# Performance work log

Hardware: AMD Instinct MI355X
Metric: run time of the kernel (lower is better)

The kernel has to match this reference:

```python
import jax, jax.numpy as jnp
import numpy as np

N = 50000   # nodes per graph
E = 1600000 # edges per graph
F = 1024    # literal feature dim (hardcoded in source)
D = 256     # gcn_dims
B = 16384   # ent_ids batch
NUM_HOPS = 3
SLOPE = 0.01  # nn.LeakyReLU default


def spmm(row, col, val, X):
    # sparse [N,N] @ X[N,F] via COO gather + segment-sum
    return jax.ops.segment_sum(val[:, None] * X[col], row, num_segments=N)


def gcn(row, col, val, X, W, b):
    return jax.nn.leaky_relu(spmm(row, col, val, X) @ W + b, SLOPE)


def setup_inputs() -> dict:
    key = jax.random.key(0)
    ks = jax.random.split(key, 24)
    d = {}
    d['ent_lit'] = jax.random.normal(ks[0], (N, F), jnp.float32)
    d['rel_lit'] = jax.random.normal(ks[1], (N, F), jnp.float32)
    d['attr_lit'] = jax.random.normal(ks[2], (N, F), jnp.float32)
    d['ent_val'] = jax.random.uniform(ks[3], (E,), jnp.float32)
    d['rel_val'] = jax.random.uniform(ks[4], (E,), jnp.float32)
    d['attr_val'] = jax.random.uniform(ks[5], (E,), jnp.float32)
    s_in = 1.0 / np.sqrt(F)
    s_d = 1.0 / np.sqrt(D)
    d['W_ent'] = jax.random.normal(ks[6], (F, D), jnp.float32) * s_in
    d['b_ent'] = jnp.zeros((D,), jnp.float32)
    d['W_rel'] = jax.random.normal(ks[7], (F, D), jnp.float32) * s_in
    d['b_rel'] = jnp.zeros((D,), jnp.float32)
    d['W_attr'] = jax.random.normal(ks[8], (F, D), jnp.float32) * s_in
    d['b_attr'] = jnp.zeros((D,), jnp.float32)
    d['W_x'] = jax.random.normal(ks[9], (D, D), jnp.float32) * s_d
    d['b_x'] = jnp.zeros((D,), jnp.float32)
    d['W_lit'] = jax.random.normal(ks[10], (F, D), jnp.float32) * s_in
    d['b_lit'] = jnp.zeros((D,), jnp.float32)
    d['W_gate'] = jax.random.normal(ks[11], (D, D), jnp.float32) * s_d
    d['b_gate'] = jnp.zeros((D,), jnp.float32)
    d['ent_row'] = jax.random.randint(ks[12], (E,), 0, N, jnp.int32)
    d['ent_col'] = jax.random.randint(ks[13], (E,), 0, N, jnp.int32)
    d['rel_row'] = jax.random.randint(ks[14], (E,), 0, N, jnp.int32)
    d['rel_col'] = jax.random.randint(ks[15], (E,), 0, N, jnp.int32)
    d['attr_row'] = jax.random.randint(ks[16], (E,), 0, N, jnp.int32)
    d['attr_col'] = jax.random.randint(ks[17], (E,), 0, N, jnp.int32)
    d['ent_ids'] = jax.random.randint(ks[18], (B,), 0, N, jnp.int32)
    return d


def reference(ent_lit, rel_lit, attr_lit, ent_val, rel_val, attr_val,
              W_ent, b_ent, W_rel, b_rel, W_attr, b_attr, W_x, b_x,
              W_lit, b_lit, W_gate, b_gate,
              ent_row, ent_col, rel_row, rel_col, attr_row, attr_col, ent_ids):
    rel_repr = gcn(rel_row, rel_col, rel_val, rel_lit, W_rel, b_rel)[ent_ids]
    attr_repr = gcn(attr_row, attr_col, attr_val, attr_lit, W_attr, b_attr)[ent_ids]
    ent_literals = ent_lit[ent_ids] @ W_lit + b_lit
    # n-hop gated aggregation
    h = gcn(ent_row, ent_col, ent_val, ent_lit, W_ent, b_ent)
    for _ in range(1, NUM_HOPS):
        nxt = jax.nn.leaky_relu(spmm(ent_row, ent_col, ent_val, h) @ W_x + b_x, SLOPE)
        g = jax.nn.sigmoid(h @ W_gate + b_gate)
        h = g * nxt + (1.0 - g) * h
    ent_n_hop = h[ent_ids]
    return jnp.concatenate([ent_literals, ent_n_hop, rel_repr, attr_repr], axis=1)
```

## Files before the change

### kernel.cpp

```cpp
#include <hip/hip_runtime.h>
#include <math.h>

#define N_NODES 50000
#define N_EDGES 1600000
#define F_DIM 1024
#define D_DIM 256
#define B_IDS 16384

#define BROWS 1024
#define BKT 49
#define NB3 (3 * BKT)
#define CHUNK 4096

typedef __attribute__((ext_vector_type(8))) short bf16x8;
typedef __attribute__((ext_vector_type(4))) float f32x4;

static inline size_t alignup(size_t x) { return (x + 255) & ~(size_t)255; }

__device__ inline unsigned short f2bf(float f) {
  unsigned u = __float_as_uint(f);
  u += 0x7fffu + ((u >> 16) & 1u);
  return (unsigned short)(u >> 16);
}
__device__ inline float bf2f(unsigned short u) {
  return __uint_as_float(((unsigned)u) << 16);
}

__device__ inline void glds16(const void* g, void* l) {
  __builtin_amdgcn_global_load_lds(
      (const __attribute__((address_space(1))) void*)g,
      (__attribute__((address_space(3))) void*)l, 16, 0, 0);
}

struct TrArgs {
  const float* W[6];
  unsigned short* Wh[6];
  unsigned short* Wl[6];
  int K[6];
};

__global__ __launch_bounds__(256) void tr_all_k(TrArgs a) {
  const int z = blockIdx.z;
  const int K = a.K[z];
  if (blockIdx.x * 64 >= K) return;
  const float* W = a.W[z];
  unsigned short* Wt_hi = a.Wh[z];
  unsigned short* Wt_lo = a.Wl[z];
  __shared__ float t[64][65];
  const int k0 = blockIdx.x * 64, n0 = blockIdx.y * 64;
  const int tid = threadIdx.x;
  const int rr = tid >> 4, c4 = (tid & 15) * 4;
#pragma unroll
  for (int q = 0; q < 4; ++q) {
    int row = q * 16 + rr;
    const float4 v = *reinterpret_cast<const float4*>(W + (size_t)(k0 + row) * 256 + n0 + c4);
    t[row][c4 + 0] = v.x; t[row][c4 + 1] = v.y; t[row][c4 + 2] = v.z; t[row][c4 + 3] = v.w;
  }
  __syncthreads();
#pragma unroll
  for (int q = 0; q < 4; ++q) {
    int n = q * 16 + rr;
    ushort4 oh, ol;
    float w0 = t[c4 + 0][n], w1 = t[c4 + 1][n], w2 = t[c4 + 2][n], w3 = t[c4 + 3][n];
    oh.x = f2bf(w0); ol.x = f2bf(w0 - bf2f(oh.x));
    oh.y = f2bf(w1); ol.y = f2bf(w1 - bf2f(oh.y));
    oh.z = f2bf(w2); ol.z = f2bf(w2 - bf2f(oh.z));
    oh.w = f2bf(w3); ol.w = f2bf(w3 - bf2f(oh.w));
    *reinterpret_cast<ushort4*>(Wt_hi + (size_t)(n0 + n) * K + k0 + c4) = oh;
    *reinterpret_cast<ushort4*>(Wt_lo + (size_t)(n0 + n) * K + k0 + c4) = ol;
  }
}


__global__ __launch_bounds__(256) void bcount_k(
    const int* __restrict__ r0, const int* __restrict__ r1, const int* __restrict__ r2,
    int* __restrict__ bcnt)
{
  __shared__ int h[NB3];
  const int t = threadIdx.x;
  for (int i = t; i < NB3; i += 256) h[i] = 0;
  __syncthreads();
  const long long cbase = (long long)blockIdx.x * CHUNK;
  const long long tot = 3LL * N_EDGES;
#pragma unroll
  for (int j = 0; j < 16; ++j) {
    long long idx = cbase + j * 256 + t;
    if (idx < tot) {
      int g = (int)(idx / N_EDGES);
      int e = (int)(idx - (long long)g * N_EDGES);
      int row = (g == 0 ? r0 : g == 1 ? r1 : r2)[e];
      atomicAdd(&h[g * BKT + (row >> 10)], 1);
    }
  }
  __syncthreads();
  for (int i = t; i < NB3; i += 256)
    if (h[i]) atomicAdd(&bcnt[i], h[i]);
}

__global__ void bscan_k(const int* __restrict__ bcnt, int* __restrict__ flatBase,
                        int* __restrict__ cursor) {
  __shared__ int c[NB3];
  const int t = threadIdx.x;
  if (t < NB3) c[t] = bcnt[t];
  __syncthreads();
  if (t < 3) {
    int acc = t * N_EDGES;
    for (int b = 0; b < BKT; ++b) {
      int i = t * BKT + b;
      int v = c[i];
      flatBase[i] = acc;
      cursor[i] = acc;
      acc += v;
    }
  }
  if (t == 0) flatBase[NB3] = 3 * N_EDGES;
}

__global__ __launch_bounds__(256) void bpart_k(
    const int* __restrict__ r0, const int* __restrict__ c0, const float* __restrict__ v0,
    const int* __restrict__ r1, const int* __restrict__ c1, const float* __restrict__ v1,
    const int* __restrict__ r2, const int* __restrict__ c2, const float* __restrict__ v2,
    int* __restrict__ cursor, int2* __restrict__ packed)
{
  __shared__ int hs[256];
  __shared__ int ls[NB3];
  __shared__ int cur[NB3];
  __shared__ int clm[NB3];
  __shared__ int2 stg[CHUNK];
  __shared__ int tgt[CHUNK];
  const int t = threadIdx.x;
  const long long cbase = (long long)blockIdx.x * CHUNK;
  const long long tot = 3LL * N_EDGES;
  hs[t] = 0;
  __syncthreads();
  int rows_[16], gbs_[16];
#pragma unroll
  for (int j = 0; j < 16; ++j) {
    long long idx = cbase + j * 256 + t;
    int gb = -1, row = 0;
    if (idx < tot) {
      int g = (int)(idx / N_EDGES);
      int e = (int)(idx - (long long)g * N_EDGES);
      row = (g == 0 ? r0 : g == 1 ? r1 : r2)[e];
      gb = g * BKT + (row >> 10);
      atomicAdd(&hs[gb], 1);
    }
    gbs_[j] = gb; rows_[j] = row;
  }
  __syncthreads();
  const int myh = hs[t];
  if (t < NB3) clm[t] = atomicAdd(&cursor[t], myh);
  for (int off = 1; off < 256; off <<= 1) {
    int v = (t >= off) ? hs[t - off] : 0;
    __syncthreads();
    hs[t] += v;
    __syncthreads();
  }
  const int excl = hs[t] - myh;
  if (t < NB3) { ls[t] = excl; cur[t] = excl; }
  __syncthreads();
#pragma unroll
  for (int j = 0; j < 16; ++j) {
    const int gb = gbs_[j];
    if (gb >= 0) {
      long long idx = cbase + j * 256 + t;
      int g = (int)(idx / N_EDGES);
      int e = (int)(idx - (long long)g * N_EDGES);
      int col = (g == 0 ? c0 : g == 1 ? c1 : c2)[e];
      float vv = (g == 0 ? v0 : g == 1 ? v1 : v2)[e];
      int slot = atomicAdd(&cur[gb], 1);
      stg[slot] = make_int2(rows_[j] | (col << 16), __float_as_int(vv));
      tgt[slot] = clm[gb] + (slot - ls[gb]);
    }
  }
  __syncthreads();
  const int cnt = (int)min((long long)CHUNK, tot - cbase);
  for (int i = t; i < cnt; i += 256) packed[tgt[i]] = stg[i];
}

__global__ __launch_bounds__(256) void bfinal_k(
    const int2* __restrict__ packed, const int* __restrict__ flatBase,
    int* __restrict__ row_ptr3, int2* __restrict__ cv3)
{
  __shared__ int hist[BROWS];
  __shared__ int part[256];
  const int gb = blockIdx.x;
  const int g = gb / BKT, b = gb % BKT;
  const int rb = b * BROWS;
  const int nrows = min(BROWS, N_NODES - rb);
  const int base = flatBase[gb];
  const int cnt = flatBase[gb + 1] - base;
  const int cvb = base - g * N_EDGES;
  const int t = threadIdx.x;
  for (int i = t; i < BROWS; i += 256) hist[i] = 0;
  __syncthreads();
  for (int i = t; i < cnt; i += 256) {
    int rc = packed[base + i].x;
    atomicAdd(&hist[(rc & 0xffff) - rb], 1);
  }
  __syncthreads();
  const int l0 = hist[4 * t], l1 = hist[4 * t + 1], l2 = hist[4 * t + 2], l3 = hist[4 * t + 3];
  const int s = l0 + l1 + l2 + l3;
  part[t] = s;
  __syncthreads();
  for (int off = 1; off < 256; off <<= 1) {
    int v = (t >= off) ? part[t - off] : 0;
    __syncthreads();
    part[t] += v;
    __syncthreads();
  }
  const int pexcl = part[t] - s;
  const int e0 = pexcl, e1 = e0 + l0, e2 = e1 + l1, e3 = e2 + l2;
  hist[4 * t] = e0; hist[4 * t + 1] = e1; hist[4 * t + 2] = e2; hist[4 * t + 3] = e3;
  int* rp = row_ptr3 + (size_t)g * (N_NODES + 1);
  if (4 * t + 0 < nrows) rp[rb + 4 * t + 0] = cvb + e0;
  if (4 * t + 1 < nrows) rp[rb + 4 * t + 1] = cvb + e1;
  if (4 * t + 2 < nrows) rp[rb + 4 * t + 2] = cvb + e2;
  if (4 * t + 3 < nrows) rp[rb + 4 * t + 3] = cvb + e3;
  if (rb + BROWS >= N_NODES && t == 0) rp[N_NODES] = N_EDGES;
  __syncthreads();
  for (int i = t; i < cnt; i += 256) {
    int2 p = packed[base + i];
    int row = p.x & 0xffff;
    int col = ((unsigned)p.x) >> 16;
    int pos = atomicAdd(&hist[row - rb], 1);
    cv3[base + pos] = make_int2(col, p.y);
  }
}

__global__ void flag_k(const int* __restrict__ ids, unsigned char* __restrict__ flag, int B) {
  int i = blockIdx.x * blockDim.x + threadIdx.x;
  if (i < B) flag[ids[i]] = 1;
}

__global__ __launch_bounds__(256) void spmm_k(
    const int* __restrict__ row_ptr, const int2* __restrict__ cv,
    const unsigned short* __restrict__ srcb, float* __restrict__ dst,
    unsigned short* __restrict__ dstb,
    const float* __restrict__ bias, int do_leaky,
    const unsigned char* __restrict__ flag, int n)
{
  int r = (blockIdx.x << 2) + (threadIdx.x >> 6);
  if (r >= n) return;
  if (flag && !flag[r]) return;
  const int lane = threadIdx.x & 63;
  const int c0 = lane << 2;
  int e0 = row_ptr[r], e1 = row_ptr[r + 1];
  float a0 = 0.f, a1 = 0.f, a2 = 0.f, a3 = 0.f;
  int e = e0;
  for (; e + 3 < e1; e += 4) {
    int2 p0 = cv[e], p1 = cv[e + 1], p2 = cv[e + 2], p3 = cv[e + 3];
    const ushort4 x0 = *reinterpret_cast<const ushort4*>(srcb + (size_t)p0.x * D_DIM + c0);
    const ushort4 x1 = *reinterpret_cast<const ushort4*>(srcb + (size_t)p1.x * D_DIM + c0);
    const ushort4 x2 = *reinterpret_cast<const ushort4*>(srcb + (size_t)p2.x * D_DIM + c0);
    const ushort4 x3 = *reinterpret_cast<const ushort4*>(srcb + (size_t)p3.x * D_DIM + c0);
    const float v0 = __int_as_float(p0.y), v1 = __int_as_float(p1.y);
    const float v2 = __int_as_float(p2.y), v3 = __int_as_float(p3.y);
    a0 = fmaf(v0, bf2f(x0.x), a0); a1 = fmaf(v0, bf2f(x0.y), a1);
    a2 = fmaf(v0, bf2f(x0.z), a2); a3 = fmaf(v0, bf2f(x0.w), a3);
    a0 = fmaf(v1, bf2f(x1.x), a0); a1 = fmaf(v1, bf2f(x1.y), a1);
    a2 = fmaf(v1, bf2f(x1.z), a2); a3 = fmaf(v1, bf2f(x1.w), a3);
    a0 = fmaf(v2, bf2f(x2.x), a0); a1 = fmaf(v2, bf2f(x2.y), a1);
    a2 = fmaf(v2, bf2f(x2.z), a2); a3 = fmaf(v2, bf2f(x2.w), a3);
    a0 = fmaf(v3, bf2f(x3.x), a0); a1 = fmaf(v3, bf2f(x3.y), a1);
    a2 = fmaf(v3, bf2f(x3.z), a2); a3 = fmaf(v3, bf2f(x3.w), a3);
  }
  for (; e < e1; ++e) {
    int2 p = cv[e];
    float v = __int_as_float(p.y);
    const ushort4 x = *reinterpret_cast<const ushort4*>(srcb + (size_t)p.x * D_DIM + c0);
    a0 = fmaf(v, bf2f(x.x), a0); a1 = fmaf(v, bf2f(x.y), a1);
    a2 = fmaf(v, bf2f(x.z), a2); a3 = fmaf(v, bf2f(x.w), a3);
  }
  if (bias) {
    const float4 b = *reinterpret_cast<const float4*>(bias + c0);
    a0 += b.x; a1 += b.y; a2 += b.z; a3 += b.w;
  }
  if (do_leaky) {
    a0 = a0 > 0.f ? a0 : 0.01f * a0;
    a1 = a1 > 0.f ? a1 : 0.01f * a1;
    a2 = a2 > 0.f ? a2 : 0.01f * a2;
    a3 = a3 > 0.f ? a3 : 0.01f * a3;
  }
  *reinterpret_cast<float4*>(dst + (size_t)r * D_DIM + c0) =
      make_float4(a0, a1, a2, a3);
  if (dstb) {
    ushort4 o;
    o.x = f2bf(a0); o.y = f2bf(a1); o.z = f2bf(a2); o.w = f2bf(a3);
    *reinterpret_cast<ushort4*>(dstb + (size_t)r * D_DIM + c0) = o;
  }
}

struct SP2 {
  const int* rp[2];
  const int2* cv[2];
  const unsigned short* src[2];
  float* dst[2];
  const float* bias[2];
};
__global__ __launch_bounds__(256) void spmm2_k(SP2 a, const unsigned char* __restrict__ flag) {
  const int z = blockIdx.y;
  int r = (blockIdx.x << 2) + (threadIdx.x >> 6);
  if (r >= N_NODES) return;
  if (!flag[r]) return;
  const unsigned short* srcb = a.src[z];
  const int lane = threadIdx.x & 63;
  const int c0 = lane << 2;
  int e0 = a.rp[z][r], e1 = a.rp[z][r + 1];
  const int2* cv = a.cv[z];
  float a0 = 0.f, a1 = 0.f, a2 = 0.f, a3 = 0.f;
  int e = e0;
  for (; e + 3 < e1; e += 4) {
    int2 p0 = cv[e], p1 = cv[e + 1], p2 = cv[e + 2], p3 = cv[e + 3];
    const ushort4 x0 = *reinterpret_cast<const ushort4*>(srcb + (size_t)p0.x * D_DIM + c0);
    const ushort4 x1 = *reinterpret_cast<const ushort4*>(srcb + (size_t)p1.x * D_DIM + c0);
    const ushort4 x2 = *reinterpret_cast<const ushort4*>(srcb + (size_t)p2.x * D_DIM + c0);
    const ushort4 x3 = *reinterpret_cast<const ushort4*>(srcb + (size_t)p3.x * D_DIM + c0);
    const float v0 = __int_as_float(p0.y), v1 = __int_as_float(p1.y);
    const float v2 = __int_as_float(p2.y), v3 = __int_as_float(p3.y);
    a0 = fmaf(v0, bf2f(x0.x), a0); a1 = fmaf(v0, bf2f(x0.y), a1);
    a2 = fmaf(v0, bf2f(x0.z), a2); a3 = fmaf(v0, bf2f(x0.w), a3);
    a0 = fmaf(v1, bf2f(x1.x), a0); a1 = fmaf(v1, bf2f(x1.y), a1);
    a2 = fmaf(v1, bf2f(x1.z), a2); a3 = fmaf(v1, bf2f(x1.w), a3);
    a0 = fmaf(v2, bf2f(x2.x), a0); a1 = fmaf(v2, bf2f(x2.y), a1);
    a2 = fmaf(v2, bf2f(x2.z), a2); a3 = fmaf(v2, bf2f(x2.w), a3);
    a0 = fmaf(v3, bf2f(x3.x), a0); a1 = fmaf(v3, bf2f(x3.y), a1);
    a2 = fmaf(v3, bf2f(x3.z), a2); a3 = fmaf(v3, bf2f(x3.w), a3);
  }
  for (; e < e1; ++e) {
    int2 p = cv[e];
    float v = __int_as_float(p.y);
    const ushort4 x = *reinterpret_cast<const ushort4*>(srcb + (size_t)p.x * D_DIM + c0);
    a0 = fmaf(v, bf2f(x.x), a0); a1 = fmaf(v, bf2f(x.y), a1);
    a2 = fmaf(v, bf2f(x.z), a2); a3 = fmaf(v, bf2f(x.w), a3);
  }
  const float4 b = *reinterpret_cast<const float4*>(a.bias[z] + c0);
  a0 += b.x; a1 += b.y; a2 += b.z; a3 += b.w;
  a0 = a0 > 0.f ? a0 : 0.01f * a0;
  a1 = a1 > 0.f ? a1 : 0.01f * a1;
  a2 = a2 > 0.f ? a2 : 0.01f * a2;
  a3 = a3 > 0.f ? a3 : 0.01f * a3;
  *reinterpret_cast<float4*>(a.dst[z] + (size_t)r * D_DIM + c0) =
      make_float4(a0, a1, a2, a3);
}

struct MM3 {
  const float* A[3];
  const unsigned short* Wh[3];
  const unsigned short* Wl[3];
  unsigned short* Cb[3];
};
__global__ __launch_bounds__(512, 4) void mm3_k(MM3 a) {
  constexpr int KT = F_DIM;
  const int z = blockIdx.y;
  const float* __restrict__ Aptr = a.A[z];
  const unsigned short* __restrict__ Wt_hi = a.Wh[z];
  const unsigned short* __restrict__ Wt_lo = a.Wl[z];
  unsigned short* __restrict__ Cb = a.Cb[z];

  __shared__ __align__(16) unsigned char smem[32768];
  const int tid = threadIdx.x;
  const int wid = tid >> 6, lane = tid & 63;
  const int wm = wid & 3, wn = wid >> 2;
  const int bm = blockIdx.x * 128;
  const int l15 = lane & 15, lk = lane >> 4;

  int mrow[2];
  const float* arow[2];
#pragma unroll
  for (int mi = 0; mi < 2; ++mi) {
    int m = bm + wm * 32 + mi * 16 + l15;
    mrow[mi] = m;
    arow[mi] = Aptr + (size_t)((m < N_NODES) ? m : 0) * KT;
  }

  const int s1 = tid, s2 = tid + 512;
  const size_t go1 = (size_t)(s1 >> 2) * KT + ((((s1 & 3) - ((s1 >> 3) & 3)) & 3) << 3);
  const size_t go2 = (size_t)(s2 >> 2) * KT + ((((s2 & 3) - ((s2 >> 3) & 3)) & 3) << 3);

  f32x4 acc[2][8] = {};
  for (int kc = 0; kc < KT / 32; ++kc) {
    const int kk = kc * 32;
    __syncthreads();
    glds16(Wt_hi + go1 + kk, smem + s1 * 16);
    glds16(Wt_hi + go2 + kk, smem + s2 * 16);
    glds16(Wt_lo + go1 + kk, smem + 16384 + s1 * 16);
    glds16(Wt_lo + go2 + kk, smem + 16384 + s2 * 16);
    const int ka = kk + lk * 8;
    bf16x8 ah[2], al[2];
#pragma unroll
    for (int mi = 0; mi < 2; ++mi) {
      bf16x8 th = {0, 0, 0, 0, 0, 0, 0, 0};
      bf16x8 tl = {0, 0, 0, 0, 0, 0, 0, 0};
      if (mrow[mi] < N_NODES) {
        const float* p = arow[mi] + ka;
        const float4 x = *reinterpret_cast<const float4*>(p);
        const float4 y = *reinterpret_cast<const float4*>(p + 4);
#define SPLIT_A(i, val) { unsigned short h_ = f2bf(val); th[i] = (short)h_; \
                          tl[i] = (short)f2bf((val) - bf2f(h_)); }
        SPLIT_A(0, x.x) SPLIT_A(1, x.y) SPLIT_A(2, x.z) SPLIT_A(3, x.w)
        SPLIT_A(4, y.x) SPLIT_A(5, y.y) SPLIT_A(6, y.z) SPLIT_A(7, y.w)
#undef SPLIT_A
      }
      ah[mi] = th; al[mi] = tl;
    }
    __syncthreads();
#pragma unroll
    for (int f = 0; f < 8; ++f) {
      const int n = wn * 128 + f * 16 + l15;
      const int boff = n * 64 + (((lk + (n >> 1)) & 3) << 4);
      const bf16x8 bh = *reinterpret_cast<const bf16x8*>(smem + boff);
      const bf16x8 bl = *reinterpret_cast<const bf16x8*>(smem + 16384 + boff);
#pragma unroll
      for (int mi = 0; mi < 2; ++mi) {
        acc[mi][f] = __builtin_amdgcn_mfma_f32_16x16x32_bf16(ah[mi], bh, acc[mi][f], 0, 0, 0);
        acc[mi][f] = __builtin_amdgcn_mfma_f32_16x16x32_bf16(al[mi], bh, acc[mi][f], 0, 0, 0);
        acc[mi][f] = __builtin_amdgcn_mfma_f32_16x16x32_bf16(ah[mi], bl, acc[mi][f], 0, 0, 0);
      }
    }
  }

#pragma unroll
  for (int mi = 0; mi < 2; ++mi) {
    const int rbase = bm + wm * 32 + mi * 16 + lk * 4;
#pragma unroll
    for (int f = 0; f < 8; ++f) {
      const int col = wn * 128 + f * 16 + l15;
#pragma unroll
      for (int r = 0; r < 4; ++r) {
        const int row = rbase + r;
        if (row >= N_NODES) continue;
        Cb[(size_t)row * D_DIM + col] = f2bf(acc[mi][f][r]);
      }
    }
  }
}

template<int KT, int MODE>
__global__ __launch_bounds__(256, 4) void mm_k(
    const float* __restrict__ Aptr,
    const unsigned short* __restrict__ Wt_hi,
    const unsigned short* __restrict__ Wt_lo,
    const float* __restrict__ bias,
    float* __restrict__ C, int ldc, int ccol0, int M,
    const int* __restrict__ rowidx,
    const float* __restrict__ nxt, const float* __restrict__ hin,
    unsigned short* __restrict__ Cb)
{
  __shared__ __align__(16) unsigned char smem[32768];
  const int tid = threadIdx.x;
  const int wid = tid >> 6, lane = tid & 63;
  const int wm = wid & 1, wn = wid >> 1;
  const int bm = blockIdx.y * 64;
  const int bn0 = blockIdx.x * 128;
  const int l15 = lane & 15, lk = lane >> 4;

  int mrow[2];
  const float* arow[2];
#pragma unroll
  for (int mi = 0; mi < 2; ++mi) {
    int m = bm + wm * 32 + mi * 16 + l15;
    mrow[mi] = m;
    int sr = (m < M) ? (rowidx ? rowidx[m] : m) : 0;
    arow[mi] = Aptr + (size_t)sr * KT;
  }

  const int st_n = tid >> 2;
  const int st_seg = ((tid & 3) - ((tid >> 3) & 3)) & 3;
  const size_t goA = (size_t)(bn0 + st_n) * KT + st_seg * 8;
  const size_t goB = goA + (size_t)64 * KT;
  const unsigned ldA = tid * 16, ldB = tid * 16 + 4096;

  f32x4 acc[2][4] = {};
  for (int kc = 0; kc < KT / 64; ++kc) {
    const int kk = kc * 64;
    __syncthreads();
    glds16(Wt_hi + goA + kk,      smem + ldA);
    glds16(Wt_hi + goB + kk,      smem + ldB);
    glds16(Wt_hi + goA + kk + 32, smem + 8192 + ldA);
    glds16(Wt_hi + goB + kk + 32, smem + 8192 + ldB);
    glds16(Wt_lo + goA + kk,      smem + 16384 + ldA);
    glds16(Wt_lo + goB + kk,      smem + 16384 + ldB);
    glds16(Wt_lo + goA + kk + 32, smem + 24576 + ldA);
    glds16(Wt_lo + goB + kk + 32, smem + 24576 + ldB);
    bf16x8 ah[2][2], al[2][2];
#pragma unroll
    for (int ks = 0; ks < 2; ++ks) {
      const int ka = kk + ks * 32 + lk * 8;
#pragma unroll
      for (int mi = 0; mi < 2; ++mi) {
        bf16x8 th = {0, 0, 0, 0, 0, 0, 0, 0};
        bf16x8 tl = {0, 0, 0, 0, 0, 0, 0, 0};
        if (mrow[mi] < M) {
          const float* p = arow[mi] + ka;
          const float4 x = *reinterpret_cast<const float4*>(p);
          const float4 y = *reinterpret_cast<const float4*>(p + 4);
#define SPLIT_A(i, val) { unsigned short h_ = f2bf(val); th[i] = (short)h_; \
                          tl[i] = (short)f2bf((val) - bf2f(h_)); }
          SPLIT_A(0, x.x) SPLIT_A(1, x.y) SPLIT_A(2, x.z) SPLIT_A(3, x.w)
          SPLIT_A(4, y.x) SPLIT_A(5, y.y) SPLIT_A(6, y.z) SPLIT_A(7, y.w)
#undef SPLIT_A
        }
        ah[ks][mi] = th; al[ks][mi] = tl;
      }
    }
    __syncthreads();
#pragma unroll
    for (int ks = 0; ks < 2; ++ks) {
#pragma unroll
      for (int f = 0; f < 4; ++f) {
        const int n = wn * 64 + f * 16 + l15;
        const int boff = ks * 8192 + n * 64 + (((lk + (n >> 1)) & 3) << 4);
        const bf16x8 bh = *reinterpret_cast<const bf16x8*>(smem + boff);
        const bf16x8 bl = *reinterpret_cast<const bf16x8*>(smem + 16384 + boff);
#pragma unroll
        for (int mi = 0; mi < 2; ++mi) {
          acc[mi][f] = __builtin_amdgcn_mfma_f32_16x16x32_bf16(ah[ks][mi], bh, acc[mi][f], 0, 0, 0);
          acc[mi][f] = __builtin_amdgcn_mfma_f32_16x16x32_bf16(al[ks][mi], bh, acc[mi][f], 0, 0, 0);
          acc[mi][f] = __builtin_amdgcn_mfma_f32_16x16x32_bf16(ah[ks][mi], bl, acc[mi][f], 0, 0, 0);
        }
      }
    }
  }

  __syncthreads();

#pragma unroll
  for (int mi = 0; mi < 2; ++mi) {
    const int rbase = bm + wm * 32 + mi * 16 + lk * 4;
    int hsrc[4];
    if (MODE == 2) {
#pragma unroll
      for (int r = 0; r < 4; ++r) {
        const int row = rbase + r;
        hsrc[r] = (rowidx && row < M) ? rowidx[row] : row;
      }
    }
#pragma unroll
    for (int f = 0; f < 4; ++f) {
      const int col = bn0 + wn * 64 + f * 16 + l15;
      const float bc = bias ? bias[col] : 0.f;
#pragma unroll
      for (int r = 0; r < 4; ++r) {
        const int row = rbase + r;
        if (row >= M) continue;
        float v = acc[mi][f][r] + bc;
        if (MODE == 1) v = v > 0.f ? v : 0.01f * v;
        if (MODE == 2) {
          const float g = 1.f / (1.f + __expf(-v));
          const float nv = nxt[(size_t)row * D_DIM + col];
          const float hv = hin[(size_t)hsrc[r] * D_DIM + col];
          v = g * nv + (1.f - g) * hv;
        }
        C[(size_t)row * ldc + ccol0 + col] = v;
        if (Cb) Cb[(size_t)row * D_DIM + col] = f2bf(v);
      }
    }
  }
}

template<int KT, int MODE>
__global__ __launch_bounds__(512, 4) void mmw_k(
    const float* __restrict__ Aptr,
    const unsigned short* __restrict__ Wt_hi,
    const unsigned short* __restrict__ Wt_lo,
    const float* __restrict__ bias,
    float* __restrict__ C, int ldc, int ccol0, int M,
    const int* __restrict__ rowidx,
    const float* __restrict__ nxt, const float* __restrict__ hin,
    unsigned short* __restrict__ Cb)
{
  __shared__ __align__(16) unsigned char smem[32768];
  const int tid = threadIdx.x;
  const int wid = tid >> 6, lane = tid & 63;
  const int wm = wid & 3, wn = wid >> 2;
  const int bm = blockIdx.x * 128;
  const int l15 = lane & 15, lk = lane >> 4;

  int mrow[2];
  const float* arow[2];
#pragma unroll
  for (int mi = 0; mi < 2; ++mi) {
    int m = bm + wm * 32 + mi * 16 + l15;
    mrow[mi] = m;
    int sr = (m < M) ? (rowidx ? rowidx[m] : m) : 0;
    arow[mi] = Aptr + (size_t)sr * KT;
  }

  const int s1 = tid, s2 = tid + 512;
  const size_t go1 = (size_t)(s1 >> 2) * KT + ((((s1 & 3) - ((s1 >> 3) & 3)) & 3) << 3);
  const size_t go2 = (size_t)(s2 >> 2) * KT + ((((s2 & 3) - ((s2 >> 3) & 3)) & 3) << 3);

  f32x4 acc[2][8] = {};
  for (int kc = 0; kc < KT / 32; ++kc) {
    const int kk = kc * 32;
    __syncthreads();
    glds16(Wt_hi + go1 + kk, smem + s1 * 16);
    glds16(Wt_hi + go2 + kk, smem + s2 * 16);
    glds16(Wt_lo + go1 + kk, smem + 16384 + s1 * 16);
    glds16(Wt_lo + go2 + kk, smem + 16384 + s2 * 16);
    const int ka = kk + lk * 8;
    bf16x8 ah[2], al[2];
#pragma unroll
    for (int mi = 0; mi < 2; ++mi) {
      bf16x8 th = {0, 0, 0, 0, 0, 0, 0, 0};
      bf16x8 tl = {0, 0, 0, 0, 0, 0, 0, 0};
      if (mrow[mi] < M) {
        const float* p = arow[mi] + ka;
        const float4 x = *reinterpret_cast<const float4*>(p);
        const float4 y = *reinterpret_cast<const float4*>(p + 4);
#define SPLIT_A(i, val) { unsigned short h_ = f2bf(val); th[i] = (short)h_; \
                          tl[i] = (short)f2bf((val) - bf2f(h_)); }
        SPLIT_A(0, x.x) SPLIT_A(1, x.y) SPLIT_A(2, x.z) SPLIT_A(3, x.w)
        SPLIT_A(4, y.x) SPLIT_A(5, y.y) SPLIT_A(6, y.z) SPLIT_A(7, y.w)
#undef SPLIT_A
      }
      ah[mi] = th; al[mi] = tl;
    }
    __syncthreads();
#pragma unroll
    for (int f = 0; f < 8; ++f) {
      const int n = wn * 128 + f * 16 + l15;
      const int boff = n * 64 + (((lk + (n >> 1)) & 3) << 4);
      const bf16x8 bh = *reinterpret_cast<const bf16x8*>(smem + boff);
      const bf16x8 bl = *reinterpret_cast<const bf16x8*>(smem + 16384 + boff);
#pragma unroll
      for (int mi = 0; mi < 2; ++mi) {
        acc[mi][f] = __builtin_amdgcn_mfma_f32_16x16x32_bf16(ah[mi], bh, acc[mi][f], 0, 0, 0);
        acc[mi][f] = __builtin_amdgcn_mfma_f32_16x16x32_bf16(al[mi], bh, acc[mi][f], 0, 0, 0);
        acc[mi][f] = __builtin_amdgcn_mfma_f32_16x16x32_bf16(ah[mi], bl, acc[mi][f], 0, 0, 0);
      }
    }
  }

  __syncthreads();

#pragma unroll
  for (int mi = 0; mi < 2; ++mi) {
    const int rbase = bm + wm * 32 + mi * 16 + lk * 4;
    int hsrc[4];
    if (MODE == 2) {
#pragma unroll
      for (int r = 0; r < 4; ++r) {
        const int row = rbase + r;
        hsrc[r] = (rowidx && row < M) ? rowidx[row] : row;
      }
    }
#pragma unroll
    for (int f = 0; f < 8; ++f) {
      const int col = wn * 128 + f * 16 + l15;
      const float bc = bias ? bias[col] : 0.f;
#pragma unroll
      for (int r = 0; r < 4; ++r) {
        const int row = rbase + r;
        if (row >= M) continue;
        float v = acc[mi][f][r] + bc;
        if (MODE == 1) v = v > 0.f ? v : 0.01f * v;
        if (MODE == 2) {
          const float g = 1.f / (1.f + __expf(-v));
          const float nv = nxt[(size_t)row * D_DIM + col];
          const float hv = hin[(size_t)hsrc[r] * D_DIM + col];
          v = g * nv + (1.f - g) * hv;
        }
        C[(size_t)row * ldc + ccol0 + col] = v;
        if (Cb) Cb[(size_t)row * D_DIM + col] = f2bf(v);
      }
    }
  }
}

__global__ __launch_bounds__(256) void gather_k(const float* __restrict__ src,
                                                const int* __restrict__ ids,
                                                float* __restrict__ dst, int ccol0, int B)
{
  int i = (blockIdx.x << 2) + (threadIdx.x >> 6);
  if (i >= B) return;
  const int lane = threadIdx.x & 63;
  const int c0 = lane << 2;
  const float4 v = *reinterpret_cast<const float4*>(src + (size_t)ids[i] * D_DIM + c0);
  *reinterpret_cast<float4*>(dst + (size_t)i * 1024 + ccol0 + c0) = v;
}

struct GA2 { const float* src[2]; int col0[2]; };
__global__ __launch_bounds__(256) void gather2_k(GA2 a, const int* __restrict__ ids,
                                                 float* __restrict__ dst)
{
  const int z = blockIdx.y;
  int i = (blockIdx.x << 2) + (threadIdx.x >> 6);
  if (i >= B_IDS) return;
  const int lane = threadIdx.x & 63;
  const int c0 = lane << 2;
  const float4 v = *reinterpret_cast<const float4*>(a.src[z] + (size_t)ids[i] * D_DIM + c0);
  *reinterpret_cast<float4*>(dst + (size_t)i * 1024 + a.col0[z] + c0) = v;
}

extern "C" void kernel_launch(void* const* d_in, const int* in_sizes, int n_in,
                              void* d_out, int out_size, void* d_ws, size_t ws_size,
                              hipStream_t stream)
{
  const float* ent_lit = (const float*)d_in[0];
  const float* rel_lit = (const float*)d_in[1];
  const float* attr_lit = (const float*)d_in[2];
  const float* ent_val = (const float*)d_in[3];
  const float* rel_val = (const float*)d_in[4];
  const float* attr_val = (const float*)d_in[5];
  const float* W_ent = (const float*)d_in[6];
  const float* b_ent = (const float*)d_in[7];
  const float* W_rel = (const float*)d_in[8];
  const float* b_rel = (const float*)d_in[9];
  const float* W_attr = (const float*)d_in[10];
  const float* b_attr = (const float*)d_in[11];
  const float* W_x = (const float*)d_in[12];
  const float* b_x = (const float*)d_in[13];
  const float* W_lit = (const float*)d_in[14];
  const float* b_lit = (const float*)d_in[15];
  const float* W_gate = (const float*)d_in[16];
  const float* b_gate = (const float*)d_in[17];
  const int* ent_row = (const int*)d_in[18];
  const int* ent_col = (const int*)d_in[19];
  const int* rel_row = (const int*)d_in[20];
  const int* rel_col = (const int*)d_in[21];
  const int* attr_row = (const int*)d_in[22];
  const int* attr_col = (const int*)d_in[23];
  const int* ent_ids = (const int*)d_in[24];
  float* out = (float*)d_out;

  char* p = (char*)d_ws;
  const size_t bufsz = alignup((size_t)N_NODES * D_DIM * 4);
  const size_t bufszb = alignup((size_t)N_NODES * D_DIM * 2);
  const size_t wsz_f = alignup((size_t)F_DIM * D_DIM * 2);
  const size_t wsz_d = alignup((size_t)D_DIM * D_DIM * 2);
  float* B0 = (float*)p; p += bufsz;
  float* B1 = (float*)p; p += bufsz;
  unsigned short* Bb0 = (unsigned short*)p; p += bufszb;
  unsigned short* Bb1 = (unsigned short*)p; p += bufszb;
  unsigned short* Bb2 = (unsigned short*)p; p += bufszb;
  float* P = (float*)Bb2;
  unsigned short* Wh_ent = (unsigned short*)p; p += wsz_f;
  unsigned short* Wl_ent = (unsigned short*)p; p += wsz_f;
  unsigned short* Wh_rel = (unsigned short*)p; p += wsz_f;
  unsigned short* Wl_rel = (unsigned short*)p; p += wsz_f;
  unsigned short* Wh_attr = (unsigned short*)p; p += wsz_f;
  unsigned short* Wl_attr = (unsigned short*)p; p += wsz_f;
  unsigned short* Wh_lit = (unsigned short*)p; p += wsz_f;
  unsigned short* Wl_lit = (unsigned short*)p; p += wsz_f;
  unsigned short* Wh_x = (unsigned short*)p; p += wsz_d;
  unsigned short* Wl_x = (unsigned short*)p; p += wsz_d;
  unsigned short* Wh_gate = (unsigned short*)p; p += wsz_d;
  unsigned short* Wl_gate = (unsigned short*)p; p += wsz_d;
  int* row_ptr3 = (int*)p; p += alignup((size_t)3 * (N_NODES + 1) * 4);
  int* bcnt = (int*)p; p += alignup((size_t)NB3 * 4);
  int* flatBase = (int*)p; p += alignup((size_t)(NB3 + 1) * 4);
  int* cursor = (int*)p; p += alignup((size_t)NB3 * 4);
  unsigned char* flags = (unsigned char*)p; p += alignup((size_t)N_NODES);
  int2* cv3 = (int2*)p; p += alignup((size_t)3 * N_EDGES * 8);
  if ((size_t)(p - (char*)d_ws) > ws_size) return;

  int2* packed = (int2*)B0;

  const int* rp_ent = row_ptr3;
  const int* rp_rel = row_ptr3 + (N_NODES + 1);
  const int* rp_attr = row_ptr3 + 2 * (N_NODES + 1);
  const int2* cv_ent = cv3;
  const int2* cv_rel = cv3 + (size_t)N_EDGES;
  const int2* cv_attr = cv3 + (size_t)2 * N_EDGES;

  dim3 blk(256), blk512(512);
  const int nchunks = (int)((3LL * N_EDGES + CHUNK - 1) / CHUNK);
  dim3 g_spmm((N_NODES + 3) / 4);
  dim3 g_spmm2((N_NODES + 3) / 4, 2);
  dim3 g_gather((B_IDS + 3) / 4);
  dim3 g_gather2((B_IDS + 3) / 4, 2);
  dim3 g_mm3((N_NODES + 127) / 128, 3);
  dim3 g_mm_ids(2, B_IDS / 64);
  dim3 g_mmw_big((N_NODES + 127) / 128);

  TrArgs ta;
  ta.W[0] = W_ent;  ta.Wh[0] = Wh_ent;  ta.Wl[0] = Wl_ent;  ta.K[0] = F_DIM;
  ta.W[1] = W_rel;  ta.Wh[1] = Wh_rel;  ta.Wl[1] = Wl_rel;  ta.K[1] = F_DIM;
  ta.W[2] = W_attr; ta.Wh[2] = Wh_attr; ta.Wl[2] = Wl_attr; ta.K[2] = F_DIM;
  ta.W[3] = W_lit;  ta.Wh[3] = Wh_lit;  ta.Wl[3] = Wl_lit;  ta.K[3] = F_DIM;
  ta.W[4] = W_x;    ta.Wh[4] = Wh_x;    ta.Wl[4] = Wl_x;    ta.K[4] = D_DIM;
  ta.W[5] = W_gate; ta.Wh[5] = Wh_gate; ta.Wl[5] = Wl_gate; ta.K[5] = D_DIM;
  tr_all_k<<<dim3(F_DIM / 64, 4, 6), blk, 0, stream>>>(ta);

  hipMemsetAsync(bcnt, 0, NB3 * sizeof(int), stream);
  bcount_k<<<dim3(nchunks), blk, 0, stream>>>(ent_row, rel_row, attr_row, bcnt);
  bscan_k<<<dim3(1), blk, 0, stream>>>(bcnt, flatBase, cursor);
  bpart_k<<<dim3(nchunks), blk, 0, stream>>>(ent_row, ent_col, ent_val,
                                             rel_row, rel_col, rel_val,
                                             attr_row, attr_col, attr_val,
                                             cursor, packed);
  bfinal_k<<<dim3(NB3), blk, 0, stream>>>(packed, flatBase, row_ptr3, cv3);

  hipMemsetAsync(flags, 0, N_NODES, stream);
  flag_k<<<dim3(B_IDS / 256), blk, 0, stream>>>(ent_ids, flags, B_IDS);

  MM3 m3;
  m3.A[0] = rel_lit;  m3.Wh[0] = Wh_rel;  m3.Wl[0] = Wl_rel;  m3.Cb[0] = Bb0;
  m3.A[1] = attr_lit; m3.Wh[1] = Wh_attr; m3.Wl[1] = Wl_attr; m3.Cb[1] = Bb1;
  m3.A[2] = ent_lit;  m3.Wh[2] = Wh_ent;  m3.Wl[2] = Wl_ent;  m3.Cb[2] = Bb2;
  mm3_k<<<g_mm3, blk512, 0, stream>>>(m3);

  SP2 s2;
  s2.rp[0] = rp_rel;  s2.cv[0] = cv_rel;  s2.src[0] = Bb0; s2.dst[0] = B1; s2.bias[0] = b_rel;
  s2.rp[1] = rp_attr; s2.cv[1] = cv_attr; s2.src[1] = Bb1; s2.dst[1] = B0; s2.bias[1] = b_attr;
  spmm2_k<<<g_spmm2, blk, 0, stream>>>(s2, flags);

  GA2 ga;
  ga.src[0] = B1; ga.col0[0] = 512;
  ga.src[1] = B0; ga.col0[1] = 768;
  gather2_k<<<g_gather2, blk, 0, stream>>>(ga, ent_ids, out);

  mm_k<F_DIM, 0><<<g_mm_ids, blk, 0, stream>>>(ent_lit, Wh_lit, Wl_lit, b_lit, out, 1024, 0,
                                               B_IDS, ent_ids, nullptr, nullptr, nullptr);

  spmm_k<<<g_spmm, blk, 0, stream>>>(rp_ent, cv_ent, Bb2, B1, Bb0, b_ent, 1, nullptr, N_NODES);
  spmm_k<<<g_spmm, blk, 0, stream>>>(rp_ent, cv_ent, Bb0, B0, nullptr, nullptr, 0, nullptr, N_NODES);
  mmw_k<D_DIM, 1><<<g_mmw_big, blk512, 0, stream>>>(B0, Wh_x, Wl_x, b_x, B0, D_DIM, 0,
                                                    N_NODES, nullptr, nullptr, nullptr, nullptr);
  mmw_k<D_DIM, 2><<<g_mmw_big, blk512, 0, stream>>>(B1, Wh_gate, Wl_gate, b_gate, B1, D_DIM, 0,
                                                    N_NODES, nullptr, B0, B1, Bb1);
  spmm_k<<<g_spmm, blk, 0, stream>>>(rp_ent, cv_ent, Bb1, B0, nullptr, nullptr, 0, flags, N_NODES);
  mm_k<D_DIM, 1><<<g_mm_ids, blk, 0, stream>>>(B0, Wh_x, Wl_x, b_x, P, D_DIM, 0,
                                               B_IDS, ent_ids, nullptr, nullptr, nullptr);
  mm_k<D_DIM, 2><<<g_mm_ids, blk, 0, stream>>>(B1, Wh_gate, Wl_gate, b_gate, out, 1024, 256,
                                               B_IDS, ent_ids, P, B1, nullptr);
}
```

Measured before the change: 1.185 ms.

## Double-buffer weight tiles and prefetch A rows in mm3 GEMM loop

Rewrites the mm3_k main loop to double-buffer the shared-memory weight tiles and to register-prefetch the next K-chunk of A rows, so global loads overlap the MFMA work on the current chunk. The plain syncthreads calls are replaced by explicit vmcnt waits plus s_barrier. Shared memory per block doubles to 64KB, which may lower occupancy under launch_bounds(512,4). The out-of-range row guard on A loads is dropped because rows are clamped to row 0, and this affects only discarded outputs. An unused gather kernel is also removed.

Result: slower. 1.407 ms (+18.7%).

```diff
diff --git a/kernel.cpp b/kernel.cpp
--- a/kernel.cpp
+++ b/kernel.cpp
@@ -352,13 +352,14 @@
 };
 __global__ __launch_bounds__(512, 4) void mm3_k(MM3 a) {
   constexpr int KT = F_DIM;
+  constexpr int NCH = KT / 32;
   const int z = blockIdx.y;
   const float* __restrict__ Aptr = a.A[z];
   const unsigned short* __restrict__ Wt_hi = a.Wh[z];
   const unsigned short* __restrict__ Wt_lo = a.Wl[z];
   unsigned short* __restrict__ Cb = a.Cb[z];
 
-  __shared__ __align__(16) unsigned char smem[32768];
+  __shared__ __align__(16) unsigned char smem[2][32768];
   const int tid = threadIdx.x;
   const int wid = tid >> 6, lane = tid & 63;
   const int wm = wid & 3, wn = wid >> 2;
@@ -378,39 +379,62 @@
   const size_t go1 = (size_t)(s1 >> 2) * KT + ((((s1 & 3) - ((s1 >> 3) & 3)) & 3) << 3);
   const size_t go2 = (size_t)(s2 >> 2) * KT + ((((s2 & 3) - ((s2 >> 3) & 3)) & 3) << 3);
 
+  float4 cx[2], cy[2];
+#pragma unroll
+  for (int mi = 0; mi < 2; ++mi) {
+    const float* p = arow[mi] + lk * 8;
+    cx[mi] = *reinterpret_cast<const float4*>(p);
+    cy[mi] = *reinterpret_cast<const float4*>(p + 4);
+  }
+  glds16(Wt_hi + go1, smem[0] + s1 * 16);
+  glds16(Wt_hi + go2, smem[0] + s2 * 16);
+  glds16(Wt_lo + go1, smem[0] + 16384 + s1 * 16);
+  glds16(Wt_lo + go2, smem[0] + 16384 + s2 * 16);
+
   f32x4 acc[2][8] = {};
-  for (int kc = 0; kc < KT / 32; ++kc) {
-    const int kk = kc * 32;
-    __syncthreads();
-    glds16(Wt_hi + go1 + kk, smem + s1 * 16);
-    glds16(Wt_hi + go2 + kk, smem + s2 * 16);
-    glds16(Wt_lo + go1 + kk, smem + 16384 + s1 * 16);
-    glds16(Wt_lo + go2 + kk, smem + 16384 + s2 * 16);
-    const int ka = kk + lk * 8;
+  for (int kc = 0; kc < NCH; ++kc) {
+    const int cur = kc & 1;
+    float4 px[2], py[2];
+    if (kc + 1 < NCH) {
+      const int ka = (kc + 1) * 32 + lk * 8;
+#pragma unroll
+      for (int mi = 0; mi < 2; ++mi) {
+        const float* p = arow[mi] + ka;
+        px[mi] = *reinterpret_cast<const float4*>(p);
+        py[mi] = *reinterpret_cast<const float4*>(p + 4);
+      }
+      const int kk = (kc + 1) * 32;
+      unsigned char* sb = smem[cur ^ 1];
+      glds16(Wt_hi + go1 + kk, sb + s1 * 16);
+      glds16(Wt_hi + go2 + kk, sb + s2 * 16);
+      glds16(Wt_lo + go1 + kk, sb + 16384 + s1 * 16);
+      glds16(Wt_lo + go2 + kk, sb + 16384 + s2 * 16);
+    }
     bf16x8 ah[2], al[2];
 #pragma unroll
     for (int mi = 0; mi < 2; ++mi) {
-      bf16x8 th = {0, 0, 0, 0, 0, 0, 0, 0};
-      bf16x8 tl = {0, 0, 0, 0, 0, 0, 0, 0};
-      if (mrow[mi] < N_NODES) {
-        const float* p = arow[mi] + ka;
-        const float4 x = *reinterpret_cast<const float4*>(p);
-        const float4 y = *reinterpret_cast<const float4*>(p + 4);
+      bf16x8 th, tl;
 #define SPLIT_A(i, val) { unsigned short h_ = f2bf(val); th[i] = (short)h_; \
                           tl[i] = (short)f2bf((val) - bf2f(h_)); }
-        SPLIT_A(0, x.x) SPLIT_A(1, x.y) SPLIT_A(2, x.z) SPLIT_A(3, x.w)
-        SPLIT_A(4, y.x) SPLIT_A(5, y.y) SPLIT_A(6, y.z) SPLIT_A(7, y.w)
+      SPLIT_A(0, cx[mi].x) SPLIT_A(1, cx[mi].y) SPLIT_A(2, cx[mi].z) SPLIT_A(3, cx[mi].w)
+      SPLIT_A(4, cy[mi].x) SPLIT_A(5, cy[mi].y) SPLIT_A(6, cy[mi].z) SPLIT_A(7, cy[mi].w)
 #undef SPLIT_A
-      }
       ah[mi] = th; al[mi] = tl;
     }
-    __syncthreads();
+    if (kc + 1 < NCH) {
+      asm volatile("s_waitcnt vmcnt(8)" ::: "memory");
+    } else {
+      asm volatile("s_waitcnt vmcnt(0)" ::: "memory");
+    }
+    __builtin_amdgcn_sched_barrier(0);
+    __builtin_amdgcn_s_barrier();
+    const unsigned char* sb = smem[cur];
 #pragma unroll
     for (int f = 0; f < 8; ++f) {
       const int n = wn * 128 + f * 16 + l15;
       const int boff = n * 64 + (((lk + (n >> 1)) & 3) << 4);
-      const bf16x8 bh = *reinterpret_cast<const bf16x8*>(smem + boff);
-      const bf16x8 bl = *reinterpret_cast<const bf16x8*>(smem + 16384 + boff);
+      const bf16x8 bh = *reinterpret_cast<const bf16x8*>(sb + boff);
+      const bf16x8 bl = *reinterpret_cast<const bf16x8*>(sb + 16384 + boff);
 #pragma unroll
       for (int mi = 0; mi < 2; ++mi) {
         acc[mi][f] = __builtin_amdgcn_mfma_f32_16x16x32_bf16(ah[mi], bh, acc[mi][f], 0, 0, 0);
@@ -418,6 +442,8 @@
         acc[mi][f] = __builtin_amdgcn_mfma_f32_16x16x32_bf16(ah[mi], bl, acc[mi][f], 0, 0, 0);
       }
     }
+    __builtin_amdgcn_s_barrier();
+    cx[0] = px[0]; cx[1] = px[1]; cy[0] = py[0]; cy[1] = py[1];
   }
 
 #pragma unroll
@@ -667,18 +693,6 @@
       }
     }
   }
-}
-
-__global__ __launch_bounds__(256) void gather_k(const float* __restrict__ src,
-                                                const int* __restrict__ ids,
-                                                float* __restrict__ dst, int ccol0, int B)
-{
-  int i = (blockIdx.x << 2) + (threadIdx.x >> 6);
-  if (i >= B) return;
-  const int lane = threadIdx.x & 63;
-  const int c0 = lane << 2;
-  const float4 v = *reinterpret_cast<const float4*>(src + (size_t)ids[i] * D_DIM + c0);
-  *reinterpret_cast<float4*>(dst + (size_t)i * 1024 + ccol0 + c0) = v;
 }
 
 struct GA2 { const float* src[2]; int col0[2]; };
@@ -769,7 +783,6 @@
   const int nchunks = (int)((3LL * N_EDGES + CHUNK - 1) / CHUNK);
   dim3 g_spmm((N_NODES + 3) / 4);
   dim3 g_spmm2((N_NODES + 3) / 4, 2);
-  dim3 g_gather((B_IDS + 3) / 4);
   dim3 g_gather2((B_IDS + 3) / 4, 2);
   dim3 g_mm3((N_NODES + 127) / 128, 3);
   dim3 g_mm_ids(2, B_IDS / 64);
```

## Double-buffer LDS and prefetch A in mm3_k to overlap loads with MFMA

Applied to the files above, without the earlier changes.

Turns the mm3_k K-loop into a two-stage software pipeline. The next chunk's A rows are loaded into registers and its weight tile is staged into a second LDS buffer while the current chunk runs its MFMAs, with explicit vmcnt waits and barriers replacing the two __syncthreads per iteration. It also removes the per-row bounds check on A (out-of-range rows now read row 0) and deletes the unused gather_k kernel. LDS use doubles to 64KB per block, which may reduce occupancy.

Result: slower. 2.600 ms (+119.4%).

```diff
diff --git a/kernel.cpp b/kernel.cpp
--- a/kernel.cpp
+++ b/kernel.cpp
@@ -352,25 +352,24 @@
 };
 __global__ __launch_bounds__(512, 4) void mm3_k(MM3 a) {
   constexpr int KT = F_DIM;
+  constexpr int NCH = KT / 32;
   const int z = blockIdx.y;
   const float* __restrict__ Aptr = a.A[z];
   const unsigned short* __restrict__ Wt_hi = a.Wh[z];
   const unsigned short* __restrict__ Wt_lo = a.Wl[z];
   unsigned short* __restrict__ Cb = a.Cb[z];
 
-  __shared__ __align__(16) unsigned char smem[32768];
+  __shared__ __align__(16) unsigned char smem[2][32768];
   const int tid = threadIdx.x;
   const int wid = tid >> 6, lane = tid & 63;
   const int wm = wid & 3, wn = wid >> 2;
   const int bm = blockIdx.x * 128;
   const int l15 = lane & 15, lk = lane >> 4;
 
-  int mrow[2];
   const float* arow[2];
 #pragma unroll
   for (int mi = 0; mi < 2; ++mi) {
     int m = bm + wm * 32 + mi * 16 + l15;
-    mrow[mi] = m;
     arow[mi] = Aptr + (size_t)((m < N_NODES) ? m : 0) * KT;
   }
 
@@ -378,47 +377,83 @@
   const size_t go1 = (size_t)(s1 >> 2) * KT + ((((s1 & 3) - ((s1 >> 3) & 3)) & 3) << 3);
   const size_t go2 = (size_t)(s2 >> 2) * KT + ((((s2 & 3) - ((s2 >> 3) & 3)) & 3) << 3);
 
+  float4 ax[2][2], ay[2][2];
+
+#define LOADA(SET, KK) {                                                     \
+    _Pragma("unroll")                                                        \
+    for (int mi = 0; mi < 2; ++mi) {                                         \
+      const float* p_ = arow[mi] + (KK) + lk * 8;                            \
+      ax[SET][mi] = *reinterpret_cast<const float4*>(p_);                    \
+      ay[SET][mi] = *reinterpret_cast<const float4*>(p_ + 4);                \
+    } }
+#define STAGE(BUF, KK) {                                                     \
+    glds16(Wt_hi + go1 + (KK), smem[BUF] + s1 * 16);                         \
+    glds16(Wt_hi + go2 + (KK), smem[BUF] + s2 * 16);                         \
+    glds16(Wt_lo + go1 + (KK), smem[BUF] + 16384 + s1 * 16);                 \
+    glds16(Wt_lo + go2 + (KK), smem[BUF] + 16384 + s2 * 16); }
+#define SPLIT1(i, val) { unsigned short h_ = f2bf(val); th[i] = (short)h_;   \
+                         tl[i] = (short)f2bf((val) - bf2f(h_)); }
+#define SPLIT(SET) {                                                         \
+    _Pragma("unroll")                                                        \
+    for (int mi = 0; mi < 2; ++mi) {                                         \
+      bf16x8 th, tl;                                                         \
+      SPLIT1(0, ax[SET][mi].x) SPLIT1(1, ax[SET][mi].y)                      \
+      SPLIT1(2, ax[SET][mi].z) SPLIT1(3, ax[SET][mi].w)                      \
+      SPLIT1(4, ay[SET][mi].x) SPLIT1(5, ay[SET][mi].y)                      \
+      SPLIT1(6, ay[SET][mi].z) SPLIT1(7, ay[SET][mi].w)                      \
+      ah[mi] = th; al[mi] = tl;                                              \
+    } }
+#define MFMA(BUF) {                                                          \
+    const unsigned char* sb_ = smem[BUF];                                    \
+    _Pragma("unroll")                                                        \
+    for (int f = 0; f < 8; ++f) {                                            \
+      const int n_ = wn * 128 + f * 16 + l15;                                \
+      const int boff_ = n_ * 64 + (((lk + (n_ >> 1)) & 3) << 4);             \
+      const bf16x8 bh_ = *reinterpret_cast<const bf16x8*>(sb_ + boff_);      \
+      const bf16x8 bl_ = *reinterpret_cast<const bf16x8*>(sb_ + 16384 + boff_); \
+      _Pragma("unroll")                                                      \
+      for (int mi = 0; mi < 2; ++mi) {                                       \
+        acc[mi][f] = __builtin_amdgcn_mfma_f32_16x16x32_bf16(ah[mi], bh_, acc[mi][f], 0, 0, 0); \
+        acc[mi][f] = __builtin_amdgcn_mfma_f32_16x16x32_bf16(al[mi], bh_, acc[mi][f], 0, 0, 0); \
+        acc[mi][f] = __builtin_amdgcn_mfma_f32_16x16x32_bf16(ah[mi], bl_, acc[mi][f], 0, 0, 0); \
+      } } }
+#define WAITK(N) { asm volatile("s_waitcnt vmcnt(" #N ")" ::: "memory");     \
+                   __builtin_amdgcn_sched_barrier(0);                        \
+                   __builtin_amdgcn_s_barrier(); }
+
+  LOADA(0, 0)
+  STAGE(0, 0)
+
   f32x4 acc[2][8] = {};
-  for (int kc = 0; kc < KT / 32; ++kc) {
-    const int kk = kc * 32;
-    __syncthreads();
-    glds16(Wt_hi + go1 + kk, smem + s1 * 16);
-    glds16(Wt_hi + go2 + kk, smem + s2 * 16);
-    glds16(Wt_lo + go1 + kk, smem + 16384 + s1 * 16);
-    glds16(Wt_lo + go2 + kk, smem + 16384 + s2 * 16);
-    const int ka = kk + lk * 8;
-    bf16x8 ah[2], al[2];
-#pragma unroll
-    for (int mi = 0; mi < 2; ++mi) {
-      bf16x8 th = {0, 0, 0, 0, 0, 0, 0, 0};
-      bf16x8 tl = {0, 0, 0, 0, 0, 0, 0, 0};
-      if (mrow[mi] < N_NODES) {
-        const float* p = arow[mi] + ka;
-        const float4 x = *reinterpret_cast<const float4*>(p);
-        const float4 y = *reinterpret_cast<const float4*>(p + 4);
-#define SPLIT_A(i, val) { unsigned short h_ = f2bf(val); th[i] = (short)h_; \
-                          tl[i] = (short)f2bf((val) - bf2f(h_)); }
-        SPLIT_A(0, x.x) SPLIT_A(1, x.y) SPLIT_A(2, x.z) SPLIT_A(3, x.w)
-        SPLIT_A(4, y.x) SPLIT_A(5, y.y) SPLIT_A(6, y.z) SPLIT_A(7, y.w)
-#undef SPLIT_A
-      }
-      ah[mi] = th; al[mi] = tl;
-    }
-    __syncthreads();
-#pragma unroll
-    for (int f = 0; f < 8; ++f) {
-      const int n = wn * 128 + f * 16 + l15;
-      const int boff = n * 64 + (((lk + (n >> 1)) & 3) << 4);
-      const bf16x8 bh = *reinterpret_cast<const bf16x8*>(smem + boff);
-      const bf16x8 bl = *reinterpret_cast<const bf16x8*>(smem + 16384 + boff);
-#pragma unroll
-      for (int mi = 0; mi < 2; ++mi) {
-        acc[mi][f] = __builtin_amdgcn_mfma_f32_16x16x32_bf16(ah[mi], bh, acc[mi][f], 0, 0, 0);
-        acc[mi][f] = __builtin_amdgcn_mfma_f32_16x16x32_bf16(al[mi], bh, acc[mi][f], 0, 0, 0);
-        acc[mi][f] = __builtin_amdgcn_mfma_f32_16x16x32_bf16(ah[mi], bl, acc[mi][f], 0, 0, 0);
-      }
-    }
-  }
+  bf16x8 ah[2], al[2];
+
+  for (int kc = 0; kc < NCH; kc += 2) {
+    LOADA(1, (kc + 1) * 32)
+    STAGE(1, (kc + 1) * 32)
+    SPLIT(0)
+    WAITK(8)
+    MFMA(0)
+    __builtin_amdgcn_s_barrier();
+    if (kc + 2 < NCH) {
+      LOADA(0, (kc + 2) * 32)
+      STAGE(0, (kc + 2) * 32)
+      SPLIT(1)
+      WAITK(8)
+      MFMA(1)
+      __builtin_amdgcn_s_barrier();
+    } else {
+      SPLIT(1)
+      WAITK(0)
+      MFMA(1)
+      __builtin_amdgcn_s_barrier();
+    }
+  }
+#undef LOADA
+#undef STAGE
+#undef SPLIT1
+#undef SPLIT
+#undef MFMA
+#undef WAITK
 
 #pragma unroll
   for (int mi = 0; mi < 2; ++mi) {
@@ -667,18 +702,6 @@
       }
     }
   }
-}
-
-__global__ __launch_bounds__(256) void gather_k(const float* __restrict__ src,
-                                                const int* __restrict__ ids,
-                                                float* __restrict__ dst, int ccol0, int B)
-{
-  int i = (blockIdx.x << 2) + (threadIdx.x >> 6);
-  if (i >= B) return;
-  const int lane = threadIdx.x & 63;
-  const int c0 = lane << 2;
-  const float4 v = *reinterpret_cast<const float4*>(src + (size_t)ids[i] * D_DIM + c0);
-  *reinterpret_cast<float4*>(dst + (size_t)i * 1024 + ccol0 + c0) = v;
 }
 
 struct GA2 { const float* src[2]; int col0[2]; };
@@ -769,7 +792,6 @@
   const int nchunks = (int)((3LL * N_EDGES + CHUNK - 1) / CHUNK);
   dim3 g_spmm((N_NODES + 3) / 4);
   dim3 g_spmm2((N_NODES + 3) / 4, 2);
-  dim3 g_gather((B_IDS + 3) / 4);
   dim3 g_gather2((B_IDS + 3) / 4, 2);
   dim3 g_mm3((N_NODES + 127) / 128, 3);
   dim3 g_mm_ids(2, B_IDS / 64);
```
